# Optimization experiments

Measured on AMD Instinct MI355X. Metric: run time of the kernel, lower is better.

## Reference

```python
import jax, jax.numpy as jnp
import numpy as np

U = 50000
I = 50000
N = U + I
D = 128
T = 3
L = 2
E = 3200000
B = 4096


def setup_inputs() -> dict:
    key = jax.random.key(0)
    ks = jax.random.split(key, 20)
    xav = lambda k, shp: jax.random.normal(k, shp, jnp.float32) * (2.0 / (shp[0] + shp[-1])) ** 0.5
    return {
        'user_indices': jax.random.randint(ks[0], (B,), 0, U, jnp.int32),
        'item_indices': jax.random.randint(ks[1], (B,), 0, I, jnp.int32),
        'edge_index': jax.random.randint(ks[2], (2, E), 0, N, jnp.int32),
        'adj_values': jax.random.uniform(ks[3], (E,), jnp.float32),
        'user_table': jax.random.normal(ks[4], (U, D), jnp.float32) * 0.01,
        'item_table': jax.random.normal(ks[5], (I, D), jnp.float32) * 0.01,
        'temporal_emb': xav(ks[6], (T, D)),
        'gcn_w': jnp.stack([xav(ks[7 + l], (D, D)) for l in range(L)]),
        'gcn_b': jnp.zeros((L, D), jnp.float32),
        'att_w1': xav(ks[9], (2 * D, D)), 'att_b1': jnp.zeros((D,), jnp.float32),
        'att_w2': xav(ks[10], (D, T)), 'att_b2': jnp.zeros((T,), jnp.float32),
        'pred_w1': xav(ks[11], (2 * D, D)), 'pred_b1': jnp.zeros((D,), jnp.float32),
        'pred_w2': xav(ks[12], (D, 1)), 'pred_b2': jnp.zeros((1,), jnp.float32),
    }


def _spmm(edge_index, adj_values, s):
    # A @ s with COO adjacency: gather src rows, scale, scatter-add to dst rows
    msgs = adj_values[:, None] * s[edge_index[1]]  # [E, D]
    return jax.ops.segment_sum(msgs, edge_index[0], num_segments=N)


def reference(user_indices, item_indices, edge_index, adj_values, user_table,
              item_table, temporal_emb, gcn_w, gcn_b, att_w1, att_b1, att_w2,
              att_b2, pred_w1, pred_b1, pred_w2, pred_b2):
    user_emb = user_table[user_indices]          # [B, D]
    item_emb = item_table[item_indices]          # [B, D]
    x = jnp.concatenate([user_table, item_table], axis=0)  # [N, D]

    temporal_outs = []
    for t in range(T):
        h = x + temporal_emb[t]
        for l in range(L):
            support = h @ gcn_w[l]
            h = jax.nn.relu(_spmm(edge_index, adj_values, support) + gcn_b[l])
        bu = h[:U][user_indices]                 # [B, D]
        bi = h[U:][item_indices]                 # [B, D]
        temporal_outs.append(jnp.concatenate([bu, bi], axis=1))
    temporal_stack = jnp.stack(temporal_outs, axis=1)  # [B, T, 2D]

    concat_orig = jnp.concatenate([user_emb, item_emb], axis=1)  # [B, 2D]
    att_h = jax.nn.relu(concat_orig @ att_w1 + att_b1)
    attn = jax.nn.softmax(att_h @ att_w2 + att_b2, axis=1)       # [B, T]
    summed = jnp.sum(temporal_stack * attn[:, :, None], axis=1)  # [B, 2D]

    ph = jax.nn.relu(summed @ pred_w1 + pred_b1)  # dropout in eval mode: identity
    pred = ph @ pred_w2 + pred_b2                 # [B, 1]
    return pred.squeeze(-1)
```

## Files before the change

kernel.cpp:

```cpp
#include <hip/hip_runtime.h>

#define U_CNT 50000
#define I_CNT 50000
#define N_NODES 100000
#define DD 128
#define T_STEPS 3
#define E_CNT 3200000
#define B_SZ 4096

#define NCOARSE 391
#define NBLK_BIN 256
#define CHUNK ((E_CNT + NBLK_BIN - 1) / NBLK_BIN)
#define SORT_CAP 10240
#define S_SCALE 256.0f
#define S_INV (1.0f / 256.0f)
#define VQ 32767.0f
#define VQ_INV (1.0f / 32767.0f)

typedef float v2f __attribute__((ext_vector_type(2)));
typedef short bf16x8 __attribute__((ext_vector_type(8)));
typedef float f32x4 __attribute__((ext_vector_type(4)));

__device__ __forceinline__ float bf2f(unsigned short u) {
    return __uint_as_float(((unsigned int)u) << 16);
}
__device__ __forceinline__ unsigned short f2bf(float f) {
    unsigned int x = __float_as_uint(f);
    x += 0x7FFF + ((x >> 16) & 1);
    return (unsigned short)(x >> 16);
}

__global__ void __launch_bounds__(256) k_bin_count(const int* __restrict__ dst,
                                                   int* __restrict__ hist) {
    __shared__ int c[NCOARSE];
    int blk = blockIdx.x, tid = threadIdx.x;
    for (int j = tid; j < NCOARSE; j += 256) c[j] = 0;
    __syncthreads();
    int s0 = blk * CHUNK, s1 = min(E_CNT, s0 + CHUNK);
    for (int i = s0 + tid; i < s1; i += 256)
        atomicAdd(&c[__builtin_nontemporal_load(&dst[i]) >> 8], 1);
    __syncthreads();
    for (int j = tid; j < NCOARSE; j += 256) hist[blk * NCOARSE + j] = c[j];
}

__global__ void __launch_bounds__(512) k_scan_a(const int* __restrict__ hist,
                                                int* __restrict__ exact_base,
                                                int* __restrict__ row_ptr) {
    __shared__ int tot[NCOARSE];
    int tid = threadIdx.x;
    for (int b = tid; b < NCOARSE; b += 512) {
        int s = 0;
        for (int blk = 0; blk < NBLK_BIN; ++blk) s += hist[blk * NCOARSE + b];
        tot[b] = s;
    }
    __syncthreads();
    if (tid == 0) {
        int run = 0;
        for (int b = 0; b < NCOARSE; ++b) {
            exact_base[b] = run;
            run += tot[b];
        }
        exact_base[NCOARSE] = run;
        row_ptr[N_NODES] = run;
    }
}

__global__ void __launch_bounds__(NBLK_BIN) k_scan_b(int* __restrict__ hist,
                                                     const int* __restrict__ exact_base) {
    __shared__ int lds[NBLK_BIN];
    int b = blockIdx.x, tid = threadIdx.x;
    int v = hist[tid * NCOARSE + b];
    lds[tid] = v;
    __syncthreads();
    for (int off = 1; off < NBLK_BIN; off <<= 1) {
        int add = (tid >= off) ? lds[tid - off] : 0;
        __syncthreads();
        lds[tid] += add;
        __syncthreads();
    }
    hist[tid * NCOARSE + b] = exact_base[b] + lds[tid] - v;
}

__global__ void __launch_bounds__(256) k_bin_scatter(const int* __restrict__ dst,
                                                     const int* __restrict__ src,
                                                     const float* __restrict__ val,
                                                     const int* __restrict__ blkbase,
                                                     int2* __restrict__ binned) {
    __shared__ int cur[NCOARSE];
    int blk = blockIdx.x, tid = threadIdx.x;
    for (int b = tid; b < NCOARSE; b += 256) cur[b] = blkbase[blk * NCOARSE + b];
    __syncthreads();
    int s0 = blk * CHUNK, s1 = min(E_CNT, s0 + CHUNK);
    for (int i = s0 + tid; i < s1; i += 256) {
        int d = __builtin_nontemporal_load(&dst[i]);
        int s = __builtin_nontemporal_load(&src[i]);
        float w = __builtin_nontemporal_load(&val[i]);
        int b = d >> 8;
        int pos = atomicAdd(&cur[b], 1);
        binned[pos] = make_int2(s | ((d & 255) << 20), __float_as_int(w));
    }
}

__global__ void __launch_bounds__(256) k_sort(const int* __restrict__ exact_base,
                                              const int2* __restrict__ binned,
                                              unsigned int* __restrict__ outp,
                                              int* __restrict__ row_ptr) {
    __shared__ int hist[256], scn[256], cur[256];
    __shared__ unsigned short perm[SORT_CAP];
    int b = blockIdx.x, tid = threadIdx.x;
    int ebase = exact_base[b];
    int cnt = exact_base[b + 1] - ebase;
    if (cnt > SORT_CAP) cnt = SORT_CAP;
    const int2* rbase = binned + ebase;
    int n0 = b << 8;
    hist[tid] = 0;
    __syncthreads();
    for (int i = tid; i < cnt; i += 256) atomicAdd(&hist[(rbase[i].x >> 20) & 255], 1);
    __syncthreads();
    scn[tid] = hist[tid];
    __syncthreads();
    for (int off = 1; off < 256; off <<= 1) {
        int v = (tid >= off) ? scn[tid - off] : 0;
        __syncthreads();
        scn[tid] += v;
        __syncthreads();
    }
    int excl = scn[tid] - hist[tid];
    cur[tid] = excl;
    if (n0 + tid < N_NODES) row_ptr[n0 + tid] = ebase + excl;
    __syncthreads();
    for (int i = tid; i < cnt; i += 256) {
        int dloc = (rbase[i].x >> 20) & 255;
        int pos = atomicAdd(&cur[dloc], 1);
        perm[pos] = (unsigned short)i;
    }
    __syncthreads();
    for (int i = tid; i < cnt; i += 256) {
        int2 p = rbase[perm[i]];
        unsigned vq = (unsigned)(__int_as_float(p.y) * VQ + 0.5f);
        outp[ebase + i] = (vq << 17) | (unsigned)(p.x & 0x1FFFF);
    }
}

__global__ void k_uvec(const float* __restrict__ temb, const float* __restrict__ w0,
                       float* __restrict__ u) {
    int k = threadIdx.x;
    for (int t = 0; t < T_STEPS; ++t) {
        float acc = 0.f;
        for (int j = 0; j < DD; ++j) acc += temb[t * DD + j] * w0[j * DD + k];
        u[t * DD + k] = acc;
    }
}

__global__ void __launch_bounds__(256) k_gemm0(const float* __restrict__ utab,
                                               const float* __restrict__ itab,
                                               const float* __restrict__ W,
                                               unsigned char* __restrict__ outf8) {
    __shared__ unsigned short wfrag[8][4][64][8];
    int tid = threadIdx.x;
    #pragma unroll
    for (int ii = 0; ii < 16; ++ii) {
        int idx = tid * 64 + ii * 4;
        int k = idx >> 7, n0 = idx & 127;
        float4 w4 = *reinterpret_cast<const float4*>(&W[idx]);
        int s = k >> 5, kb = (k >> 3) & 3, j = k & 7;
        float wv[4] = {w4.x, w4.y, w4.z, w4.w};
        #pragma unroll
        for (int m = 0; m < 4; ++m) {
            int n = n0 + m;
            wfrag[n >> 4][s][(n & 15) | (kb << 4)][j] = f2bf(wv[m]);
        }
    }
    __syncthreads();
    int lane = tid & 63, wid = tid >> 6;
    int r16 = lane & 15, kb = lane >> 4;
    const int ntiles = (N_NODES + 63) / 64;
    for (int tile = blockIdx.x; tile < ntiles; tile += gridDim.x) {
        int wbase = tile * 64 + wid * 16;
        int row = wbase + r16;
        bool ok = row < N_NODES;
        const float* xrow = ok ? ((row < U_CNT) ? &utab[(size_t)row * DD]
                                                : &itab[(size_t)(row - U_CNT) * DD])
                               : &utab[0];
        bf16x8 afrag[4];
        #pragma unroll
        for (int s = 0; s < 4; ++s) {
            float4 a0, a1;
            if (ok) {
                a0 = *reinterpret_cast<const float4*>(&xrow[s * 32 + kb * 8]);
                a1 = *reinterpret_cast<const float4*>(&xrow[s * 32 + kb * 8 + 4]);
            } else {
                a0 = make_float4(0.f, 0.f, 0.f, 0.f);
                a1 = a0;
            }
            afrag[s][0] = (short)f2bf(a0.x);
            afrag[s][1] = (short)f2bf(a0.y);
            afrag[s][2] = (short)f2bf(a0.z);
            afrag[s][3] = (short)f2bf(a0.w);
            afrag[s][4] = (short)f2bf(a1.x);
            afrag[s][5] = (short)f2bf(a1.y);
            afrag[s][6] = (short)f2bf(a1.z);
            afrag[s][7] = (short)f2bf(a1.w);
        }
        #pragma unroll
        for (int c = 0; c < 8; ++c) {
            f32x4 acc = {0.f, 0.f, 0.f, 0.f};
            #pragma unroll
            for (int s = 0; s < 4; ++s) {
                bf16x8 bfrag = *reinterpret_cast<bf16x8*>(&wfrag[c][s][lane][0]);
                acc = __builtin_amdgcn_mfma_f32_16x16x32_bf16(afrag[s], bfrag, acc, 0, 0, 0);
            }
            int orow0 = wbase + (lane >> 4) * 4;
            int ocol = c * 16 + (lane & 15);
            #pragma unroll
            for (int r = 0; r < 4; ++r) {
                int orow = orow0 + r;
                if (orow < N_NODES) {
                    unsigned pk = __builtin_amdgcn_cvt_pk_fp8_f32(acc[r] * S_SCALE,
                                                                  acc[r] * S_SCALE, 0, false);
                    outf8[(size_t)orow * DD + ocol] = (unsigned char)(pk & 0xFF);
                }
            }
        }
    }
}

__global__ void __launch_bounds__(256) k_spmm_full(const int* __restrict__ row_ptr,
                                                   const unsigned int* __restrict__ pack,
                                                   const unsigned char* __restrict__ Sf,
                                                   unsigned short* __restrict__ Pb,
                                                   float* __restrict__ rvec) {
    int wave = (int)((blockIdx.x * blockDim.x + threadIdx.x) >> 6);
    int lane = threadIdx.x & 63;
    if (wave >= N_NODES) return;
    int beg = row_ptr[wave], end = row_ptr[wave + 1];
    int q = lane >> 3;
    int cg = lane & 7;
    v2f acc[8];
    #pragma unroll
    for (int j = 0; j < 8; ++j) acc[j] = (v2f){0.f, 0.f};
    float vs = 0.f;
    int e0 = beg + q;
    unsigned pl = (e0 < end) ? __builtin_nontemporal_load(&pack[e0]) : 0u;
    for (int e = beg; e < end; e += 8) {
        unsigned cur = pl;
        int en = e + 8 + q;
        pl = (en < end) ? __builtin_nontemporal_load(&pack[en]) : 0u;
        int sx = (int)(cur & 0x1FFFF);
        float v = (float)(cur >> 17) * VQ_INV;
        const int4 s4 = *reinterpret_cast<const int4*>(&Sf[((size_t)sx << 7) + (cg << 4)]);
        v2f vv = {v, v};
        acc[0] += vv * __builtin_amdgcn_cvt_pk_f32_fp8(s4.x, false);
        acc[1] += vv * __builtin_amdgcn_cvt_pk_f32_fp8(s4.x, true);
        acc[2] += vv * __builtin_amdgcn_cvt_pk_f32_fp8(s4.y, false);
        acc[3] += vv * __builtin_amdgcn_cvt_pk_f32_fp8(s4.y, true);
        acc[4] += vv * __builtin_amdgcn_cvt_pk_f32_fp8(s4.z, false);
        acc[5] += vv * __builtin_amdgcn_cvt_pk_f32_fp8(s4.z, true);
        acc[6] += vv * __builtin_amdgcn_cvt_pk_f32_fp8(s4.w, false);
        acc[7] += vv * __builtin_amdgcn_cvt_pk_f32_fp8(s4.w, true);
        if (cg == 0) vs += v;
    }
    float out[16];
    #pragma unroll
    for (int j = 0; j < 8; ++j) {
        out[2 * j] = acc[j].x;
        out[2 * j + 1] = acc[j].y;
    }
    #pragma unroll
    for (int j = 0; j < 16; ++j) {
        out[j] += __shfl_down(out[j], 32, 64);
        out[j] += __shfl_down(out[j], 16, 64);
        out[j] += __shfl_down(out[j], 8, 64);
        out[j] *= S_INV;
    }
    vs += __shfl_down(vs, 32, 64);
    vs += __shfl_down(vs, 16, 64);
    vs += __shfl_down(vs, 8, 64);
    if (lane < 8) {
        unsigned w0 = ((unsigned)f2bf(out[1]) << 16) | f2bf(out[0]);
        unsigned w1 = ((unsigned)f2bf(out[3]) << 16) | f2bf(out[2]);
        unsigned w2 = ((unsigned)f2bf(out[5]) << 16) | f2bf(out[4]);
        unsigned w3 = ((unsigned)f2bf(out[7]) << 16) | f2bf(out[6]);
        unsigned w4 = ((unsigned)f2bf(out[9]) << 16) | f2bf(out[8]);
        unsigned w5 = ((unsigned)f2bf(out[11]) << 16) | f2bf(out[10]);
        unsigned w6 = ((unsigned)f2bf(out[13]) << 16) | f2bf(out[12]);
        unsigned w7 = ((unsigned)f2bf(out[15]) << 16) | f2bf(out[14]);
        unsigned short* base = &Pb[((size_t)wave << 7) + (lane << 4)];
        *reinterpret_cast<int4*>(base) = make_int4(w0, w1, w2, w3);
        *reinterpret_cast<int4*>(base + 8) = make_int4(w4, w5, w6, w7);
        if (lane == 0) rvec[wave] = vs;
    }
}

__global__ void __launch_bounds__(256) k_spmm_out3(const int* __restrict__ row_ptr,
                                                   const unsigned int* __restrict__ pack,
                                                   const unsigned short* __restrict__ Pb,
                                                   const float* __restrict__ rvec,
                                                   const int* __restrict__ uidx,
                                                   const int* __restrict__ iidx,
                                                   const float* __restrict__ uvec,
                                                   const float* __restrict__ b0,
                                                   float* __restrict__ agg) {
    int slot = (int)((blockIdx.x * blockDim.x + threadIdx.x) >> 6);
    int lane = threadIdx.x & 63;
    if (slot >= 2 * B_SZ) return;
    int b = slot & (B_SZ - 1), side = slot >> 12;
    int row = side ? (U_CNT + iidx[b]) : uidx[b];
    int beg = row_ptr[row], end = row_ptr[row + 1];
    int half = lane >> 5, cg = lane & 31;
    float u0[4], u1[4], u2[4], bb[4];
    #pragma unroll
    for (int j = 0; j < 4; ++j) {
        int c = cg * 4 + j;
        u0[j] = uvec[c];
        u1[j] = uvec[DD + c];
        u2[j] = uvec[2 * DD + c];
        bb[j] = b0[c];
    }
    float a0[4] = {0, 0, 0, 0}, a1[4] = {0, 0, 0, 0}, a2[4] = {0, 0, 0, 0};
    for (int e = beg; e < end; e += 2) {
        int ee = e + half;
        unsigned pw = (ee < end) ? __builtin_nontemporal_load(&pack[ee]) : 0u;
        int sx = (int)(pw & 0x1FFFF);
        float v = (float)(pw >> 17) * VQ_INV;
        float rr = rvec[sx];
        ushort4 s4 = *reinterpret_cast<const ushort4*>(&Pb[(size_t)sx * DD + cg * 4]);
        float pc[4] = {bf2f(s4.x), bf2f(s4.y), bf2f(s4.z), bf2f(s4.w)};
        #pragma unroll
        for (int j = 0; j < 4; ++j) {
            float base = pc[j] + bb[j];
            a0[j] += v * fmaxf(base + rr * u0[j], 0.f);
            a1[j] += v * fmaxf(base + rr * u1[j], 0.f);
            a2[j] += v * fmaxf(base + rr * u2[j], 0.f);
        }
    }
    #pragma unroll
    for (int j = 0; j < 4; ++j) {
        a0[j] += __shfl_down(a0[j], 32, 64);
        a1[j] += __shfl_down(a1[j], 32, 64);
        a2[j] += __shfl_down(a2[j], 32, 64);
    }
    if (lane < 32) {
        size_t rb = (size_t)slot * 3;
        float4 o0 = {a0[0], a0[1], a0[2], a0[3]};
        float4 o1 = {a1[0], a1[1], a1[2], a1[3]};
        float4 o2 = {a2[0], a2[1], a2[2], a2[3]};
        *reinterpret_cast<float4*>(&agg[(rb + 0) * DD + lane * 4]) = o0;
        *reinterpret_cast<float4*>(&agg[(rb + 1) * DD + lane * 4]) = o1;
        *reinterpret_cast<float4*>(&agg[(rb + 2) * DD + lane * 4]) = o2;
    }
}

__global__ void __launch_bounds__(256) k_head(const float* __restrict__ agg,
                                              const float* __restrict__ W,
                                              const float* __restrict__ b1,
                                              float* __restrict__ tstack) {
    __shared__ unsigned short wfrag[8][4][64][8];
    __shared__ float blds[DD];
    int tid = threadIdx.x;
    #pragma unroll
    for (int ii = 0; ii < 16; ++ii) {
        int idx = tid * 64 + ii * 4;
        int k = idx >> 7, n0 = idx & 127;
        float4 w4 = *reinterpret_cast<const float4*>(&W[idx]);
        int s = k >> 5, kb = (k >> 3) & 3, j = k & 7;
        float wv[4] = {w4.x, w4.y, w4.z, w4.w};
        #pragma unroll
        for (int m = 0; m < 4; ++m) {
            int n = n0 + m;
            wfrag[n >> 4][s][(n & 15) | (kb << 4)][j] = f2bf(wv[m]);
        }
    }
    if (tid < DD) blds[tid] = b1[tid];
    __syncthreads();
    int lane = tid & 63, wid = tid >> 6;
    int r16 = lane & 15, kb = lane >> 4;
    const int NR = 2 * B_SZ * T_STEPS;
    const int ntiles = NR / 64;
    for (int tile = blockIdx.x; tile < ntiles; tile += gridDim.x) {
        int wbase = tile * 64 + wid * 16;
        int row = wbase + r16;
        const float* arow = &agg[(size_t)row * DD];
        bf16x8 afrag[4];
        #pragma unroll
        for (int s = 0; s < 4; ++s) {
            float4 a0 = *reinterpret_cast<const float4*>(&arow[s * 32 + kb * 8]);
            float4 a1 = *reinterpret_cast<const float4*>(&arow[s * 32 + kb * 8 + 4]);
            afrag[s][0] = (short)f2bf(a0.x);
            afrag[s][1] = (short)f2bf(a0.y);
            afrag[s][2] = (short)f2bf(a0.z);
            afrag[s][3] = (short)f2bf(a0.w);
            afrag[s][4] = (short)f2bf(a1.x);
            afrag[s][5] = (short)f2bf(a1.y);
            afrag[s][6] = (short)f2bf(a1.z);
            afrag[s][7] = (short)f2bf(a1.w);
        }
        #pragma unroll
        for (int c = 0; c < 8; ++c) {
            f32x4 acc = {0.f, 0.f, 0.f, 0.f};
            #pragma unroll
            for (int s = 0; s < 4; ++s) {
                bf16x8 bfrag = *reinterpret_cast<bf16x8*>(&wfrag[c][s][lane][0]);
                acc = __builtin_amdgcn_mfma_f32_16x16x32_bf16(afrag[s], bfrag, acc, 0, 0, 0);
            }
            int orow0 = wbase + (lane >> 4) * 4;
            int ocol = c * 16 + (lane & 15);
            float bb = blds[ocol];
            #pragma unroll
            for (int r = 0; r < 4; ++r) {
                int orow = orow0 + r;
                int slot = orow / 3, t = orow - slot * 3;
                int bi = slot & (B_SZ - 1), side = slot >> 12;
                float o = fmaxf(acc[r] + bb, 0.f);
                tstack[((size_t)bi * T_STEPS + t) * 2 * DD + side * DD + ocol] = o;
            }
        }
    }
}

__global__ void __launch_bounds__(128) k_final(const int* __restrict__ uidx,
                                               const int* __restrict__ iidx,
                                               const float* __restrict__ utab,
                                               const float* __restrict__ itab,
                                               const float* __restrict__ aw1,
                                               const float* __restrict__ ab1,
                                               const float* __restrict__ aw2,
                                               const float* __restrict__ ab2,
                                               const float* __restrict__ pw1,
                                               const float* __restrict__ pb1,
                                               const float* __restrict__ pw2,
                                               const float* __restrict__ pb2,
                                               const float* __restrict__ tstack,
                                               float* __restrict__ outp) {
    __shared__ float s[2 * DD];
    __shared__ float ah[DD];
    __shared__ float attn[T_STEPS];
    __shared__ float summed[2 * DD];
    __shared__ float red[2];
    int b = blockIdx.x, tid = threadIdx.x;
    int u = uidx[b], it = iidx[b];
    s[tid] = utab[(size_t)u * DD + tid];
    s[tid + DD] = itab[(size_t)it * DD + tid];
    __syncthreads();
    float acc = ab1[tid];
    for (int k = 0; k < 2 * DD; ++k) acc += s[k] * aw1[k * DD + tid];
    ah[tid] = fmaxf(acc, 0.f);
    __syncthreads();
    if (tid < T_STEPS) {
        float lg = ab2[tid];
        for (int k = 0; k < DD; ++k) lg += ah[k] * aw2[k * T_STEPS + tid];
        attn[tid] = lg;
    }
    __syncthreads();
    if (tid == 0) {
        float m = fmaxf(attn[0], fmaxf(attn[1], attn[2]));
        float e0 = expf(attn[0] - m), e1 = expf(attn[1] - m), e2 = expf(attn[2] - m);
        float inv = 1.f / (e0 + e1 + e2);
        attn[0] = e0 * inv;
        attn[1] = e1 * inv;
        attn[2] = e2 * inv;
    }
    __syncthreads();
    const float* tb = &tstack[(size_t)b * T_STEPS * 2 * DD];
    for (int k = tid; k < 2 * DD; k += 128)
        summed[k] = attn[0] * tb[k] + attn[1] * tb[2 * DD + k] + attn[2] * tb[4 * DD + k];
    __syncthreads();
    float ph = pb1[tid];
    for (int k = 0; k < 2 * DD; ++k) ph += summed[k] * pw1[k * DD + tid];
    ph = fmaxf(ph, 0.f);
    float contrib = ph * pw2[tid];
    for (int off = 32; off > 0; off >>= 1) contrib += __shfl_down(contrib, off, 64);
    if ((tid & 63) == 0) red[tid >> 6] = contrib;
    __syncthreads();
    if (tid == 0) outp[b] = red[0] + red[1] + pb2[0];
}

extern "C" void kernel_launch(void* const* d_in, const int* in_sizes, int n_in,
                              void* d_out, int out_size, void* d_ws, size_t ws_size,
                              hipStream_t stream) {
    const int* uidx = (const int*)d_in[0];
    const int* iidx = (const int*)d_in[1];
    const int* eidx = (const int*)d_in[2];
    const float* adj = (const float*)d_in[3];
    const float* utab = (const float*)d_in[4];
    const float* itab = (const float*)d_in[5];
    const float* temb = (const float*)d_in[6];
    const float* gw = (const float*)d_in[7];
    const float* gb = (const float*)d_in[8];
    const float* aw1 = (const float*)d_in[9];
    const float* ab1 = (const float*)d_in[10];
    const float* aw2 = (const float*)d_in[11];
    const float* ab2 = (const float*)d_in[12];
    const float* pw1 = (const float*)d_in[13];
    const float* pb1 = (const float*)d_in[14];
    const float* pw2 = (const float*)d_in[15];
    const float* pb2 = (const float*)d_in[16];

    char* ws = (char*)d_ws;
    size_t off = 0;
    auto alloc = [&](size_t bytes) {
        void* p = ws + off;
        off += (bytes + 255) & ~(size_t)255;
        return p;
    };
    int* hist = (int*)alloc((size_t)NBLK_BIN * NCOARSE * 4);
    int* exact_base = (int*)alloc((NCOARSE + 1) * 4);
    int* row_ptr = (int*)alloc((size_t)(N_NODES + 1) * 4);
    unsigned int* sorted = (unsigned int*)alloc((size_t)E_CNT * 4);
    float* rvec = (float*)alloc((size_t)N_NODES * 4);
    float* uvec = (float*)alloc((size_t)T_STEPS * DD * 4);
    void* un = alloc((size_t)E_CNT * 8);
    int2* binned = (int2*)un;
    unsigned char* Sf = (unsigned char*)un;
    unsigned short* Pb = (unsigned short*)alloc((size_t)N_NODES * DD * 2);
    float* agg = (float*)alloc((size_t)2 * B_SZ * T_STEPS * DD * 4);
    float* tstack = (float*)alloc((size_t)B_SZ * T_STEPS * 2 * DD * 4);

    k_bin_count<<<NBLK_BIN, 256, 0, stream>>>(eidx, hist);
    k_scan_a<<<1, 512, 0, stream>>>(hist, exact_base, row_ptr);
    k_scan_b<<<NCOARSE, NBLK_BIN, 0, stream>>>(hist, exact_base);
    k_bin_scatter<<<NBLK_BIN, 256, 0, stream>>>(eidx, eidx + E_CNT, adj, hist, binned);
    k_sort<<<NCOARSE, 256, 0, stream>>>(exact_base, binned, sorted, row_ptr);
    k_gemm0<<<512, 256, 0, stream>>>(utab, itab, gw, Sf);
    k_uvec<<<1, DD, 0, stream>>>(temb, gw, uvec);
    k_spmm_full<<<(N_NODES + 3) / 4, 256, 0, stream>>>(row_ptr, sorted, Sf, Pb, rvec);
    k_spmm_out3<<<(2 * B_SZ * 64) / 256, 256, 0, stream>>>(row_ptr, sorted, Pb, rvec,
                                                           uidx, iidx, uvec, gb, agg);
    k_head<<<384, 256, 0, stream>>>(agg, gw + DD * DD, gb + DD, tstack);
    k_final<<<B_SZ, 128, 0, stream>>>(uidx, iidx, utab, itab, aw1, ab1, aw2, ab2, pw1,
                                      pb1, pw2, pb2, tstack, (float*)d_out);
}
```

Baseline: 306.6 us.

## Stage GEMM input tiles via swizzled LDS and batch rows in final head

The two MFMA GEMM kernels (k_gemm0 and k_head) now load each 64-row input tile into shared memory with coalesced float4 reads, convert to bf16, and store with an XOR swizzle. Fragments are then read back as bf16x8 vectors, replacing the previous strided per-lane global loads. k_final now processes 8 batch rows per 256-thread block, so each weight element read from global memory is reused across four rows per thread instead of once per block. This costs extra shared memory and syncs per tile, and k_final launches fewer, larger blocks.

```diff
diff --git a/kernel.cpp b/kernel.cpp
--- a/kernel.cpp
+++ b/kernel.cpp
@@ -16,6 +16,7 @@
 #define S_INV (1.0f / 256.0f)
 #define VQ 32767.0f
 #define VQ_INV (1.0f / 32767.0f)
+#define FB 8
 
 typedef float v2f __attribute__((ext_vector_type(2)));
 typedef short bf16x8 __attribute__((ext_vector_type(8)));
@@ -157,6 +158,7 @@
                                                const float* __restrict__ W,
                                                unsigned char* __restrict__ outf8) {
     __shared__ unsigned short wfrag[8][4][64][8];
+    __shared__ unsigned short xs[64 * 128];
     int tid = threadIdx.x;
     #pragma unroll
     for (int ii = 0; ii < 16; ++ii) {
@@ -171,37 +173,36 @@
             wfrag[n >> 4][s][(n & 15) | (kb << 4)][j] = f2bf(wv[m]);
         }
     }
-    __syncthreads();
     int lane = tid & 63, wid = tid >> 6;
-    int r16 = lane & 15, kb = lane >> 4;
     const int ntiles = (N_NODES + 63) / 64;
     for (int tile = blockIdx.x; tile < ntiles; tile += gridDim.x) {
-        int wbase = tile * 64 + wid * 16;
-        int row = wbase + r16;
-        bool ok = row < N_NODES;
-        const float* xrow = ok ? ((row < U_CNT) ? &utab[(size_t)row * DD]
-                                                : &itab[(size_t)(row - U_CNT) * DD])
-                               : &utab[0];
+        __syncthreads();
+        int tbase = tile * 64;
+        #pragma unroll
+        for (int p = 0; p < 8; ++p) {
+            int idx = p * 1024 + tid * 4;
+            int row = idx >> 7, c = idx & 127;
+            int grow = tbase + row;
+            float4 a = make_float4(0.f, 0.f, 0.f, 0.f);
+            if (grow < N_NODES) {
+                const float* src = (grow < U_CNT) ? &utab[(size_t)grow * DD + c]
+                                                  : &itab[(size_t)(grow - U_CNT) * DD + c];
+                a = *reinterpret_cast<const float4*>(src);
+            }
+            int si = (row * 128 + c) ^ ((row & 7) << 3);
+            ushort4 o = {f2bf(a.x), f2bf(a.y), f2bf(a.z), f2bf(a.w)};
+            *reinterpret_cast<ushort4*>(&xs[si]) = o;
+        }
+        __syncthreads();
+        int rowt = wid * 16 + (lane & 15);
+        int kb = lane >> 4;
         bf16x8 afrag[4];
         #pragma unroll
         for (int s = 0; s < 4; ++s) {
-            float4 a0, a1;
-            if (ok) {
-                a0 = *reinterpret_cast<const float4*>(&xrow[s * 32 + kb * 8]);
-                a1 = *reinterpret_cast<const float4*>(&xrow[s * 32 + kb * 8 + 4]);
-            } else {
-                a0 = make_float4(0.f, 0.f, 0.f, 0.f);
-                a1 = a0;
-            }
-            afrag[s][0] = (short)f2bf(a0.x);
-            afrag[s][1] = (short)f2bf(a0.y);
-            afrag[s][2] = (short)f2bf(a0.z);
-            afrag[s][3] = (short)f2bf(a0.w);
-            afrag[s][4] = (short)f2bf(a1.x);
-            afrag[s][5] = (short)f2bf(a1.y);
-            afrag[s][6] = (short)f2bf(a1.z);
-            afrag[s][7] = (short)f2bf(a1.w);
-        }
+            int si = (rowt * 128 + s * 32 + kb * 8) ^ ((rowt & 7) << 3);
+            afrag[s] = *reinterpret_cast<bf16x8*>(&xs[si]);
+        }
+        int wbase = tbase + wid * 16;
         #pragma unroll
         for (int c = 0; c < 8; ++c) {
             f32x4 acc = {0.f, 0.f, 0.f, 0.f};
@@ -356,6 +357,7 @@
                                               const float* __restrict__ b1,
                                               float* __restrict__ tstack) {
     __shared__ unsigned short wfrag[8][4][64][8];
+    __shared__ unsigned short xs[64 * 128];
     __shared__ float blds[DD];
     int tid = threadIdx.x;
     #pragma unroll
@@ -372,29 +374,31 @@
         }
     }
     if (tid < DD) blds[tid] = b1[tid];
-    __syncthreads();
     int lane = tid & 63, wid = tid >> 6;
-    int r16 = lane & 15, kb = lane >> 4;
     const int NR = 2 * B_SZ * T_STEPS;
     const int ntiles = NR / 64;
     for (int tile = blockIdx.x; tile < ntiles; tile += gridDim.x) {
-        int wbase = tile * 64 + wid * 16;
-        int row = wbase + r16;
-        const float* arow = &agg[(size_t)row * DD];
+        __syncthreads();
+        int tbase = tile * 64;
+        #pragma unroll
+        for (int p = 0; p < 8; ++p) {
+            int idx = p * 1024 + tid * 4;
+            int row = idx >> 7, c = idx & 127;
+            float4 a = *reinterpret_cast<const float4*>(&agg[(size_t)(tbase + row) * DD + c]);
+            int si = (row * 128 + c) ^ ((row & 7) << 3);
+            ushort4 o = {f2bf(a.x), f2bf(a.y), f2bf(a.z), f2bf(a.w)};
+            *reinterpret_cast<ushort4*>(&xs[si]) = o;
+        }
+        __syncthreads();
+        int rowt = wid * 16 + (lane & 15);
+        int kb = lane >> 4;
         bf16x8 afrag[4];
         #pragma unroll
         for (int s = 0; s < 4; ++s) {
-            float4 a0 = *reinterpret_cast<const float4*>(&arow[s * 32 + kb * 8]);
-            float4 a1 = *reinterpret_cast<const float4*>(&arow[s * 32 + kb * 8 + 4]);
-            afrag[s][0] = (short)f2bf(a0.x);
-            afrag[s][1] = (short)f2bf(a0.y);
-            afrag[s][2] = (short)f2bf(a0.z);
-            afrag[s][3] = (short)f2bf(a0.w);
-            afrag[s][4] = (short)f2bf(a1.x);
-            afrag[s][5] = (short)f2bf(a1.y);
-            afrag[s][6] = (short)f2bf(a1.z);
-            afrag[s][7] = (short)f2bf(a1.w);
-        }
+            int si = (rowt * 128 + s * 32 + kb * 8) ^ ((rowt & 7) << 3);
+            afrag[s] = *reinterpret_cast<bf16x8*>(&xs[si]);
+        }
+        int wbase = tbase + wid * 16;
         #pragma unroll
         for (int c = 0; c < 8; ++c) {
             f32x4 acc = {0.f, 0.f, 0.f, 0.f};
@@ -418,7 +422,7 @@
     }
 }
 
-__global__ void __launch_bounds__(128) k_final(const int* __restrict__ uidx,
+__global__ void __launch_bounds__(256) k_final(const int* __restrict__ uidx,
                                                const int* __restrict__ iidx,
                                                const float* __restrict__ utab,
                                                const float* __restrict__ itab,
@@ -432,47 +436,85 @@
                                                const float* __restrict__ pb2,
                                                const float* __restrict__ tstack,
                                                float* __restrict__ outp) {
-    __shared__ float s[2 * DD];
-    __shared__ float ah[DD];
-    __shared__ float attn[T_STEPS];
-    __shared__ float summed[2 * DD];
-    __shared__ float red[2];
-    int b = blockIdx.x, tid = threadIdx.x;
-    int u = uidx[b], it = iidx[b];
-    s[tid] = utab[(size_t)u * DD + tid];
-    s[tid + DD] = itab[(size_t)it * DD + tid];
-    __syncthreads();
-    float acc = ab1[tid];
-    for (int k = 0; k < 2 * DD; ++k) acc += s[k] * aw1[k * DD + tid];
-    ah[tid] = fmaxf(acc, 0.f);
-    __syncthreads();
-    if (tid < T_STEPS) {
-        float lg = ab2[tid];
-        for (int k = 0; k < DD; ++k) lg += ah[k] * aw2[k * T_STEPS + tid];
-        attn[tid] = lg;
-    }
-    __syncthreads();
-    if (tid == 0) {
-        float m = fmaxf(attn[0], fmaxf(attn[1], attn[2]));
-        float e0 = expf(attn[0] - m), e1 = expf(attn[1] - m), e2 = expf(attn[2] - m);
+    __shared__ float s[FB][2 * DD];
+    __shared__ float ah[FB][DD];
+    __shared__ float attn[FB][4];
+    __shared__ float summed[FB][2 * DD];
+    __shared__ float red[FB][DD];
+    __shared__ int uu[FB], ii[FB];
+    int b0 = blockIdx.x * FB, tid = threadIdx.x;
+    if (tid < FB) {
+        uu[tid] = uidx[b0 + tid];
+        ii[tid] = iidx[b0 + tid];
+    }
+    __syncthreads();
+    #pragma unroll
+    for (int r = 0; r < FB; ++r)
+        s[r][tid] = (tid < DD) ? utab[(size_t)uu[r] * DD + tid]
+                               : itab[(size_t)ii[r] * DD + (tid - DD)];
+    __syncthreads();
+    {
+        int c = tid & 127, g = tid >> 7;
+        float acc0 = ab1[c], acc1 = acc0, acc2 = acc0, acc3 = acc0;
+        for (int k = 0; k < 2 * DD; ++k) {
+            float w = aw1[k * DD + c];
+            acc0 += s[g][k] * w;
+            acc1 += s[g + 2][k] * w;
+            acc2 += s[g + 4][k] * w;
+            acc3 += s[g + 6][k] * w;
+        }
+        ah[g][c] = fmaxf(acc0, 0.f);
+        ah[g + 2][c] = fmaxf(acc1, 0.f);
+        ah[g + 4][c] = fmaxf(acc2, 0.f);
+        ah[g + 6][c] = fmaxf(acc3, 0.f);
+    }
+    __syncthreads();
+    if (tid < FB * T_STEPS) {
+        int r = tid / 3, t = tid - r * 3;
+        float lg = ab2[t];
+        for (int k = 0; k < DD; ++k) lg += ah[r][k] * aw2[k * T_STEPS + t];
+        attn[r][t] = lg;
+    }
+    __syncthreads();
+    if (tid < FB) {
+        float m = fmaxf(attn[tid][0], fmaxf(attn[tid][1], attn[tid][2]));
+        float e0 = expf(attn[tid][0] - m), e1 = expf(attn[tid][1] - m),
+              e2 = expf(attn[tid][2] - m);
         float inv = 1.f / (e0 + e1 + e2);
-        attn[0] = e0 * inv;
-        attn[1] = e1 * inv;
-        attn[2] = e2 * inv;
-    }
-    __syncthreads();
-    const float* tb = &tstack[(size_t)b * T_STEPS * 2 * DD];
-    for (int k = tid; k < 2 * DD; k += 128)
-        summed[k] = attn[0] * tb[k] + attn[1] * tb[2 * DD + k] + attn[2] * tb[4 * DD + k];
-    __syncthreads();
-    float ph = pb1[tid];
-    for (int k = 0; k < 2 * DD; ++k) ph += summed[k] * pw1[k * DD + tid];
-    ph = fmaxf(ph, 0.f);
-    float contrib = ph * pw2[tid];
-    for (int off = 32; off > 0; off >>= 1) contrib += __shfl_down(contrib, off, 64);
-    if ((tid & 63) == 0) red[tid >> 6] = contrib;
-    __syncthreads();
-    if (tid == 0) outp[b] = red[0] + red[1] + pb2[0];
+        attn[tid][0] = e0 * inv;
+        attn[tid][1] = e1 * inv;
+        attn[tid][2] = e2 * inv;
+    }
+    __syncthreads();
+    #pragma unroll
+    for (int r = 0; r < FB; ++r) {
+        const float* tb = &tstack[(size_t)(b0 + r) * T_STEPS * 2 * DD];
+        summed[r][tid] =
+            attn[r][0] * tb[tid] + attn[r][1] * tb[2 * DD + tid] + attn[r][2] * tb[4 * DD + tid];
+    }
+    __syncthreads();
+    {
+        int c = tid & 127, g = tid >> 7;
+        float p0 = pb1[c], p1 = p0, p2 = p0, p3 = p0;
+        for (int k = 0; k < 2 * DD; ++k) {
+            float w = pw1[k * DD + c];
+            p0 += summed[g][k] * w;
+            p1 += summed[g + 2][k] * w;
+            p2 += summed[g + 4][k] * w;
+            p3 += summed[g + 6][k] * w;
+        }
+        float wc = pw2[c];
+        red[g][c] = fmaxf(p0, 0.f) * wc;
+        red[g + 2][c] = fmaxf(p1, 0.f) * wc;
+        red[g + 4][c] = fmaxf(p2, 0.f) * wc;
+        red[g + 6][c] = fmaxf(p3, 0.f) * wc;
+    }
+    __syncthreads();
+    if (tid < FB) {
+        float sum = pb2[0];
+        for (int k = 0; k < DD; ++k) sum += red[tid][k];
+        outp[b0 + tid] = sum;
+    }
 }
 
 extern "C" void kernel_launch(void* const* d_in, const int* in_sizes, int n_in,
@@ -527,6 +569,6 @@
     k_spmm_out3<<<(2 * B_SZ * 64) / 256, 256, 0, stream>>>(row_ptr, sorted, Pb, rvec,
                                                            uidx, iidx, uvec, gb, agg);
     k_head<<<384, 256, 0, stream>>>(agg, gw + DD * DD, gb + DD, tstack);
-    k_final<<<B_SZ, 128, 0, stream>>>(uidx, iidx, utab, itab, aw1, ab1, aw2, ab2, pw1,
-                                      pb1, pw2, pb2, tstack, (float*)d_out);
-}
+    k_final<<<B_SZ / FB, 256, 0, stream>>>(uidx, iidx, utab, itab, aw1, ab1, aw2, ab2,
+                                           pw1, pb1, pw2, pb2, tstack, (float*)d_out);
+}
```

New measurement: 303.7 us. Within noise of the previous version (-0.9%).
